# Kernel tuning notes

Measured on AMD Instinct MI355X. Metric: run time of the kernel, lower is better.

Reference implementation:

```python
import jax, jax.numpy as jnp
import numpy as np

NEG = -9e15
EPS = 1e-5

# GraphAttention (classic GAT layer): h = xW; e_ij = LeakyReLU(a1.h_i + a2.h_j);
# attention = softmax(where(adj>0, e, -9e15)); out = attention @ h.
# The torch code builds one big block-diagonal adjacency; off-block entries get
# -9e15 and underflow to exactly 0 after softmax, so batched per-block GAT is
# numerically identical and avoids the O((B*N)^2) dense waste.

def gat(x, adj, W, a1, a2):
    h = jnp.einsum('bnf,fh->bnh', x, W)
    e = jax.nn.leaky_relu(jnp.einsum('bnh,h->bn', h, a1)[:, :, None]
                          + jnp.einsum('bnh,h->bn', h, a2)[:, None, :], 0.2)
    att = jax.nn.softmax(jnp.where(adj > 0, e, NEG), axis=-1)
    return jnp.einsum('bnm,bmh->bnh', att, h)

def mlp(x, W1, b1, W2, b2):
    return jax.nn.relu(x @ W1 + b1) @ W2 + b2


def setup_inputs() -> dict:
    key = jax.random.key(0)
    ks = iter(jax.random.split(key, 40))
    B, NV, NO = 8, 500, 1500
    DV, DO, H = 512, 32, 128

    def mat(din, dout):
        return jax.random.normal(next(ks), (din, dout), jnp.float32) / np.sqrt(din)

    def vec(d):
        return jax.random.normal(next(ks), (d,), jnp.float32) * 0.1

    inp = {
        'vis_memory': jax.random.normal(next(ks), (B, NV, DV), jnp.float32),
        'obj_memory': jax.random.normal(next(ks), (B, NO, DO), jnp.float32),
        'vis_adj': jax.random.uniform(next(ks), (B, NV, NV), jnp.float32),
        'obj_adj': jax.random.uniform(next(ks), (B, NO, NO), jnp.float32),
        'object_A_OV': jax.random.uniform(next(ks), (B, NO, NV), jnp.float32),
        # GAT layers
        'Wv1': mat(DV, H), 'av1a': vec(H), 'av1b': vec(H),
        'Wv2': mat(H, H),  'av2a': vec(H), 'av2b': vec(H),
        'Wo1': mat(DO, H), 'ao1a': vec(H), 'ao1b': vec(H),
        'Wo2': mat(H, H),  'ao2a': vec(H), 'ao2b': vec(H),
        # globalTobject / objectTglobal MLPs
        'g2o_W1': mat(H, H), 'g2o_b1': jnp.zeros((H,), jnp.float32),
        'g2o_W2': mat(H, H), 'g2o_b2': jnp.zeros((H,), jnp.float32),
        'o2g_W1': mat(H, H), 'o2g_b1': jnp.zeros((H,), jnp.float32),
        'o2g_W2': mat(H, H), 'o2g_b2': jnp.zeros((H,), jnp.float32),
        # output projections
        'img_W': mat(H, DV), 'img_b': jnp.zeros((DV,), jnp.float32),
        'obj_W': mat(H, DO), 'obj_b': jnp.zeros((DO,), jnp.float32),
    }
    return inp


def reference(vis_memory, obj_memory, vis_adj, obj_adj, object_A_OV,
              Wv1, av1a, av1b, Wv2, av2a, av2b,
              Wo1, ao1a, ao1b, Wo2, ao2a, ao2b,
              g2o_W1, g2o_b1, g2o_W2, g2o_b2,
              o2g_W1, o2g_b1, o2g_W2, o2g_b2,
              img_W, img_b, obj_W, obj_b):
    # cross adjacencies (block-diagonal in torch -> batched here)
    vo = jnp.swapaxes(object_A_OV, 1, 2)            # (B, NV, NO)
    vo = vo / (vo.sum(2, keepdims=True) + EPS)
    ov = jnp.swapaxes(vo, 1, 2)                     # (B, NO, NV)
    ov = ov / (ov.sum(2, keepdims=True) + EPS)

    v1 = jax.nn.relu(gat(vis_memory, vis_adj, Wv1, av1a, av1b))
    o1 = jax.nn.relu(gat(obj_memory, obj_adj, Wo1, ao1a, ao1b))
    vis = v1 + mlp(jnp.einsum('bvo,boh->bvh', vo, o1), o2g_W1, o2g_b1, o2g_W2, o2g_b2)
    obj = o1 + mlp(jnp.einsum('bov,bvh->boh', ov, v1), g2o_W1, g2o_b1, g2o_W2, g2o_b2)

    v2 = jax.nn.relu(gat(vis, vis_adj, Wv2, av2a, av2b))
    o2 = jax.nn.relu(gat(obj, obj_adj, Wo2, ao2a, ao2b))
    vis = v2 + mlp(jnp.einsum('bvo,boh->bvh', vo, o2), o2g_W1, o2g_b1, o2g_W2, o2g_b2)
    obj = o2 + mlp(jnp.einsum('bov,bvh->boh', ov, v2), g2o_W1, g2o_b1, g2o_W2, g2o_b2)

    vis_out = vis @ img_W + img_b                   # (B, NV, DV)
    obj_out = obj @ obj_W + obj_b                   # (B, NO, DO)
    return (vis_out, obj_out)
```

## Files before the change

### kernel.cpp

```cpp
#include <hip/hip_runtime.h>
#include <math.h>

#define EPSV 1e-5f
#define HD 128
#define IT 64
#define JT 32
#define WP 68
#define CCH 16
#define THR 256

typedef __attribute__((address_space(3))) uint32_t lds_u32_t;
typedef __attribute__((address_space(1))) uint32_t gbl_u32_t;
typedef __attribute__((ext_vector_type(8))) short bf16x8;
typedef __attribute__((ext_vector_type(4))) float f32x4;

__device__ __forceinline__ void async_copy16(const float* g, float* l) {
    __builtin_amdgcn_global_load_lds((const gbl_u32_t*)g, (lds_u32_t*)l, 16, 0, 0);
}

__device__ __forceinline__ void stage_tile_async(const float* gsrc, float* lds, int t) {
    int wv = t >> 6, lane = t & 63;
#pragma unroll
    for (int it = 0; it < 4; ++it) {
        int c = it * 4 + wv;
        async_copy16(gsrc + c * 256 + lane * 4, lds + c * 256);
    }
}

__device__ __forceinline__ void stage_8k_128(const void* g, void* l, int t) {
    const float* gf = (const float*)g; float* lf = (float*)l;
    async_copy16(gf + t * 4, lf + t * 4);
    async_copy16(gf + t * 4 + 512, lf + t * 4 + 512);
    async_copy16(gf + t * 4 + 1024, lf + t * 4 + 1024);
    async_copy16(gf + t * 4 + 1536, lf + t * 4 + 1536);
}

__device__ __forceinline__ unsigned int f2bf(float f) {
    return __builtin_bit_cast(unsigned int, f) >> 16;
}

__device__ __forceinline__ unsigned short rne_bf16(float f) {
    unsigned int u = __builtin_bit_cast(unsigned int, f);
    u += 0x7FFFu + ((u >> 16) & 1u);
    return (unsigned short)(u >> 16);
}

struct WprepP { const float *W, *a1, *a2; unsigned short* WT; float *wa1, *wa2; int K; };
struct XprepP { const float* X; unsigned short* Xbf; const float *wa1, *wa2;
                float *sa, *sb; int rows; };
struct GmfP   { const unsigned short *Xbf, *WT; unsigned short* hT; int N, tilesJ; };
struct AggP  { const unsigned int* mask; const float *sa, *sb, *sm; const unsigned short* hT;
               float* out; int N, tiles, tilesJ; };
struct CrossP{ const float *A, *src, *rs1; float *pp; int iN, jN, tiles, tps; };
struct MlpP  { const float *pp, *scale; int S; const float *W1, *b1, *W2, *b2, *res;
               float *out; int rows; };


__global__ void colsum_part_k(const float* __restrict__ A, float* __restrict__ s1p,
                              int B, int NO, int NV) {
    int v = blockIdx.x * 256 + threadIdx.x;
    int c = blockIdx.y, b = blockIdx.z;
    if (v >= NV) return;
    int chunk = (NO + CCH - 1) / CCH;
    int o0 = c * chunk;
    int o1 = o0 + chunk; if (o1 > NO) o1 = NO;
    const float* Ab = A + (size_t)b * NO * NV + v;
    float s = 0.f;
    for (int o = o0; o < o1; ++o) s += Ab[(size_t)o * NV];
    s1p[((size_t)b * CCH + c) * NV + v] = s;
}

__global__ void colsum_fin_k(const float* __restrict__ s1p, float* __restrict__ rs1,
                             int B, int NV) {
    int idx = blockIdx.x * 256 + threadIdx.x;
    if (idx >= B * NV) return;
    int b = idx / NV, v = idx - b * NV;
    float s = 0.f;
    for (int c = 0; c < CCH; ++c) s += s1p[((size_t)b * CCH + c) * NV + v];
    rs1[idx] = 1.f / (s + EPSV);
}

__global__ void rowsum_inv_k(const float* __restrict__ A, const float* __restrict__ rs1,
                             float* __restrict__ rs2, int B, int NO, int NV) {
    int row = blockIdx.x * (blockDim.x >> 6) + (threadIdx.x >> 6);
    int lane = threadIdx.x & 63;
    if (row >= B * NO) return;
    int b = row / NO;
    const float* Ar = A + (size_t)row * NV;
    const float* r1 = rs1 + (size_t)b * NV;
    float s = 0.f;
    for (int v = lane; v < NV; v += 64) s += Ar[v] * r1[v];
    for (int off = 32; off; off >>= 1) s += __shfl_xor(s, off, 64);
    if (lane == 0) rs2[row] = 1.f / (s + EPSV);
}

template<int N, int TILESJ>
__global__ __launch_bounds__(256)
void maskg_k(const float* __restrict__ adj, unsigned int* __restrict__ maskT) {
    int tid = blockIdx.x * 256 + threadIdx.x;
    int w = tid % TILESJ;
    int rowid = tid / TILESJ;
    if (rowid >= 8 * N) return;
    int b = rowid / N, i = rowid - b * N;
    int j0 = w * 32;
    const float* src = adj + (size_t)rowid * N + j0;
    unsigned int bits = 0u;
    if (j0 + 32 <= N) {
#pragma unroll
        for (int q = 0; q < 8; ++q) {
            float4 v = ((const float4*)src)[q];
            bits |= (v.x > 0.f ? 1u : 0u) << (q * 4 + 0);
            bits |= (v.y > 0.f ? 1u : 0u) << (q * 4 + 1);
            bits |= (v.z > 0.f ? 1u : 0u) << (q * 4 + 2);
            bits |= (v.w > 0.f ? 1u : 0u) << (q * 4 + 3);
        }
    } else {
#pragma unroll
        for (int r = 0; r < 32; ++r)
            if (j0 + r < N) bits |= (src[r] > 0.f ? 1u : 0u) << r;
    }
    maskT[((size_t)b * TILESJ + w) * N + i] = bits;
}

__global__ __launch_bounds__(256)
void wprep_k(WprepP p0, WprepP p1, WprepP p2, WprepP p3, int e0, int e1, int e2) {
    __shared__ float lw[32][129];
    __shared__ float a1s[128], a2s[128];
    int bid = blockIdx.x;
    const WprepP& P = bid < e0 ? p0 : bid < e1 ? p1 : bid < e2 ? p2 : p3;
    int lb = bid < e0 ? bid : bid < e1 ? bid - e0 : bid < e2 ? bid - e1 : bid - e2;
    int k0 = lb * 32, K = P.K;
    int t = threadIdx.x;
    if (t < 128) { a1s[t] = P.a1[t]; a2s[t] = P.a2[t]; }
    for (int idx = t; idx < 32 * 32; idx += 256) {
        int kk = idx >> 5, c4 = idx & 31;
        float4 v = ((const float4*)(P.W + (size_t)(k0 + kk) * 128))[c4];
        lw[kk][c4 * 4 + 0] = v.x; lw[kk][c4 * 4 + 1] = v.y;
        lw[kk][c4 * 4 + 2] = v.z; lw[kk][c4 * 4 + 3] = v.w;
    }
    __syncthreads();
    int kk = t >> 3, g = t & 7;
    float s1 = 0.f, s2 = 0.f;
    for (int c = g; c < 128; c += 8) {
        float w = lw[kk][c];
        s1 = fmaf(w, a1s[c], s1);
        s2 = fmaf(w, a2s[c], s2);
    }
    s1 += __shfl_xor(s1, 1, 64); s1 += __shfl_xor(s1, 2, 64); s1 += __shfl_xor(s1, 4, 64);
    s2 += __shfl_xor(s2, 1, 64); s2 += __shfl_xor(s2, 2, 64); s2 += __shfl_xor(s2, 4, 64);
    if (g == 0) { P.wa1[k0 + kk] = s1; P.wa2[k0 + kk] = s2; }
    for (int idx = t; idx < 4096; idx += 256) {
        int c = idx >> 5, k = idx & 31;
        P.WT[(size_t)c * K + k0 + k] = rne_bf16(lw[k][c]);
    }
}

template<int K>
__device__ void xprep_body(const XprepP& P, int lb) {
    int t = threadIdx.x, wv = t >> 6, lane = t & 63;
    int row = lb * 4 + wv;
    if (row >= P.rows) return;
    const float4* x4 = (const float4*)(P.X + (size_t)row * K);
    const float4* w14 = (const float4*)P.wa1;
    const float4* w24 = (const float4*)P.wa2;
    unsigned short* xb = P.Xbf + (size_t)row * K;
    float s1 = 0.f, s2 = 0.f;
    constexpr int K4 = K / 4;
    constexpr int NI = (K4 + 63) / 64;
#pragma unroll
    for (int i = 0; i < NI; ++i) {
        int k4 = i * 64 + lane;
        if ((K4 % 64 == 0) || (k4 < K4)) {
            float4 x = x4[k4];
            float4 a = w14[k4];
            float4 b = w24[k4];
            s1 += x.x * a.x + x.y * a.y + x.z * a.z + x.w * a.w;
            s2 += x.x * b.x + x.y * b.y + x.z * b.z + x.w * b.w;
            ushort4 p = make_ushort4(rne_bf16(x.x), rne_bf16(x.y),
                                     rne_bf16(x.z), rne_bf16(x.w));
            *(ushort4*)(xb + (size_t)k4 * 4) = p;
        }
    }
#pragma unroll
    for (int off = 32; off; off >>= 1) {
        s1 += __shfl_xor(s1, off, 64);
        s2 += __shfl_xor(s2, off, 64);
    }
    if (lane == 0) { P.sa[row] = s1; P.sb[row] = s2; }
}

template<int KV, int KO>
__global__ __launch_bounds__(256)
void xprep2_k(XprepP V, XprepP O, int GV) {
    int bid = blockIdx.x;
    if (bid < GV) xprep_body<KV>(V, bid);
    else          xprep_body<KO>(O, bid - GV);
}

template<int K>
__device__ void gmf_body(const GmfP& P, int lb) {
    int tilesJ = P.tilesJ, N = P.N;
    int b = lb / tilesJ, jt = lb - b * tilesJ;
    int t = threadIdx.x, wv = t >> 6, lane = t & 63;
    int ml = lane & 15, quad = lane >> 4;
    const unsigned short* xb = P.Xbf + ((size_t)b * N + (size_t)jt * 32) * K;
    const unsigned short* wt0 = P.WT + (size_t)(wv * 32 + ml) * K;
    const unsigned short* wt1 = wt0 + (size_t)16 * K;
    const unsigned short* xb0 = xb + (size_t)ml * K;
    const unsigned short* xb1 = xb + (size_t)(16 + ml) * K;
    f32x4 acc00 = {0.f, 0.f, 0.f, 0.f}, acc01 = acc00, acc10 = acc00, acc11 = acc00;
#pragma unroll 4
    for (int kt = 0; kt < K / 32; ++kt) {
        int kk = kt * 32 + quad * 8;
        bf16x8 a0 = *(const bf16x8*)(wt0 + kk);
        bf16x8 a1 = *(const bf16x8*)(wt1 + kk);
        bf16x8 b0 = *(const bf16x8*)(xb0 + kk);
        bf16x8 b1 = *(const bf16x8*)(xb1 + kk);
        acc00 = __builtin_amdgcn_mfma_f32_16x16x32_bf16(a0, b0, acc00, 0, 0, 0);
        acc01 = __builtin_amdgcn_mfma_f32_16x16x32_bf16(a0, b1, acc01, 0, 0, 0);
        acc10 = __builtin_amdgcn_mfma_f32_16x16x32_bf16(a1, b0, acc10, 0, 0, 0);
        acc11 = __builtin_amdgcn_mfma_f32_16x16x32_bf16(a1, b1, acc11, 0, 0, 0);
    }
    unsigned short* hb = P.hT + (size_t)(b * tilesJ + jt) * 4096;
    int nvalid = N - jt * 32; if (nvalid > 32) nvalid = 32;
    bool ok0 = ml < nvalid, ok1 = (16 + ml) < nvalid;
    int c0 = wv * 32 + quad * 4;
#pragma unroll
    for (int r = 0; r < 4; ++r) {
        int ca = c0 + r, cb = c0 + 16 + r;
        int swa = ((ca >> 1) & 3) << 3, swb = ((cb >> 1) & 3) << 3;
        hb[ca * 32 + (ml ^ swa)]        = ok0 ? rne_bf16(acc00[r]) : 0;
        hb[ca * 32 + ((16 + ml) ^ swa)] = ok1 ? rne_bf16(acc01[r]) : 0;
        hb[cb * 32 + (ml ^ swb)]        = ok0 ? rne_bf16(acc10[r]) : 0;
        hb[cb * 32 + ((16 + ml) ^ swb)] = ok1 ? rne_bf16(acc11[r]) : 0;
    }
}

template<int KV, int KO>
__global__ __launch_bounds__(256)
void gmf2_k(GmfP V, GmfP O, int GV) {
    int bid = blockIdx.x;
    if (bid < GV) gmf_body<KV>(V, bid);
    else          gmf_body<KO>(O, bid - GV);
}

__global__ __launch_bounds__(256)
void sbmax2_k(const float* __restrict__ sbV, float* __restrict__ smV,
              const float* __restrict__ sbO, float* __restrict__ smO,
              int NV, int NO) {
    __shared__ float red[256];
    int b0 = blockIdx.x, t = threadIdx.x;
    const float* sb; float* out; int N;
    if (b0 < 8) { sb = sbV + (size_t)b0 * NV; out = smV + b0; N = NV; }
    else        { sb = sbO + (size_t)(b0 - 8) * NO; out = smO + (b0 - 8); N = NO; }
    float m = -INFINITY;
    for (int j = t; j < N; j += 256) m = fmaxf(m, sb[j]);
    red[t] = m; __syncthreads();
    for (int s = 128; s; s >>= 1) {
        if (t < s) red[t] = fmaxf(red[t], red[t + s]);
        __syncthreads();
    }
    if (t == 0) *out = red[0];
}

struct SharedAgg32 {
    unsigned short hsT[5][128][32];
    unsigned int mask_s[48][32];
    float sb_s[48 * 32];
    float z_s[32];
};

__device__ void agg_body(SharedAgg32& sm, const AggP& P, int lbid) {
    int tiles = P.tiles;
    int b = lbid / tiles;
    int i0 = (lbid - b * tiles) * 32;
    int N = P.N, T = P.tilesJ;
    int t = threadIdx.x;
    int wv = t >> 6, lane = t & 63, quad = lane >> 4, ml = lane & 15;
    const unsigned int* mb = P.mask + (size_t)b * T * N + i0;
    for (int idx = t; idx < T * 8; idx += 128) {
        int w = idx >> 3, r4 = idx & 7;
        *(uint4*)&sm.mask_s[w][r4 * 4] = *(const uint4*)&mb[(size_t)w * N + r4 * 4];
    }
    const float* sbb = P.sb + (size_t)b * N;
    for (int idx = t; idx < T * 8; idx += 128)
        ((float4*)sm.sb_s)[idx] = ((const float4*)sbb)[idx];
    int row_loc = wv * 16 + ml;
    int irow = i0 + row_loc;
    float sa = (irow < N) ? P.sa[(size_t)b * N + irow] : 0.f;
    float e0 = sa + P.sm[b];
    float m = e0 > 0.f ? e0 : 0.2f * e0;
    __syncthreads();
    const unsigned short* hTb = P.hT + (size_t)b * T * 4096;
    stage_8k_128(hTb, &sm.hsT[0][0][0], t);
    if (T > 1) stage_8k_128(hTb + 4096, &sm.hsT[1][0][0], t);
    if (T > 2) stage_8k_128(hTb + 8192, &sm.hsT[2][0][0], t);
    if (T > 3) stage_8k_128(hTb + 12288, &sm.hsT[3][0][0], t);

    int nq2 = (quad ^ ((ml >> 1) & 3)) * 8;
    f32x4 acc[8];
#pragma unroll
    for (int nt = 0; nt < 8; ++nt)
#pragma unroll
        for (int r = 0; r < 4; ++r) acc[nt][r] = 0.f;
    float zacc = 0.f;
    for (int tt = 0; tt < T; ++tt) {
        int cur = tt - (tt / 5) * 5;
        unsigned int mq = sm.mask_s[tt][row_loc] >> (quad * 8);
        float4 s0 = *(const float4*)&sm.sb_s[tt * 32 + quad * 8];
        float4 s1 = *(const float4*)&sm.sb_s[tt * 32 + quad * 8 + 4];
        float sv[8] = {s0.x, s0.y, s0.z, s0.w, s1.x, s1.y, s1.z, s1.w};
        float w_[8];
#pragma unroll
        for (int i = 0; i < 8; ++i) {
            float e = sa + sv[i];
            e = e > 0.f ? e : 0.2f * e;
            float ww = __expf(e - m);
            ww = ((mq >> i) & 1u) ? ww : 0.f;
            zacc += ww;
            w_[i] = ww;
        }
        unsigned int u0 = f2bf(w_[0]) | (__builtin_bit_cast(unsigned int, w_[1]) & 0xFFFF0000u);
        unsigned int u1 = f2bf(w_[2]) | (__builtin_bit_cast(unsigned int, w_[3]) & 0xFFFF0000u);
        unsigned int u2 = f2bf(w_[4]) | (__builtin_bit_cast(unsigned int, w_[5]) & 0xFFFF0000u);
        unsigned int u3 = f2bf(w_[6]) | (__builtin_bit_cast(unsigned int, w_[7]) & 0xFFFF0000u);
        uint4 af = make_uint4(u0, u1, u2, u3);
        bf16x8 afrag = __builtin_bit_cast(bf16x8, af);
        int rem = T - tt;
        if (rem >= 4)      asm volatile("s_waitcnt vmcnt(12)" ::: "memory");
        else if (rem == 3) asm volatile("s_waitcnt vmcnt(8)" ::: "memory");
        else if (rem == 2) asm volatile("s_waitcnt vmcnt(4)" ::: "memory");
        else               asm volatile("s_waitcnt vmcnt(0)" ::: "memory");
        __builtin_amdgcn_s_barrier();
        asm volatile("" ::: "memory");
        if (tt + 4 < T) {
            int nb = tt + 4; nb -= (nb / 5) * 5;
            stage_8k_128(hTb + (size_t)(tt + 4) * 4096, &sm.hsT[nb][0][0], t);
        }
#pragma unroll
        for (int nt = 0; nt < 8; ++nt) {
            bf16x8 bfrag = *(const bf16x8*)&sm.hsT[cur][nt * 16 + ml][nq2];
            acc[nt] = __builtin_amdgcn_mfma_f32_16x16x32_bf16(afrag, bfrag, acc[nt], 0, 0, 0);
        }
    }
    zacc += __shfl_xor(zacc, 16, 64);
    zacc += __shfl_xor(zacc, 32, 64);
    if (quad == 0) sm.z_s[row_loc] = zacc;
    __syncthreads();
    float* outb = P.out + (size_t)b * N * HD;
#pragma unroll
    for (int r = 0; r < 4; ++r) {
        int rr = wv * 16 + quad * 4 + r;
        float inv = 1.f / sm.z_s[rr];
        int row = i0 + rr;
        if (row < N) {
#pragma unroll
            for (int nt = 0; nt < 8; ++nt)
                outb[(size_t)row * HD + nt * 16 + ml] = fmaxf(acc[nt][r] * inv, 0.f);
        }
    }
}

__global__ __launch_bounds__(128)
void agg2_k(AggP V, AggP O, int GVb) {
    __shared__ SharedAgg32 sm;
    int bid = blockIdx.x;
    if (bid < GVb) agg_body(sm, V, bid);
    else           agg_body(sm, O, bid - GVb);
}

__device__ __forceinline__ void tile_fma256(const float (*hs)[HD], const float (*ws)[WP],
                                            int rg, int c0, float acc[4][8]) {
#pragma unroll 8
    for (int jl = 0; jl < JT; ++jl) {
        float4 h0 = *(const float4*)&hs[jl][c0];
        float4 h1 = *(const float4*)&hs[jl][c0 + 64];
        float4 w4 = *(const float4*)&ws[jl][rg * 4];
        float wq[4] = {w4.x, w4.y, w4.z, w4.w};
#pragma unroll
        for (int q = 0; q < 4; ++q) {
            float w = wq[q];
            acc[q][0] = fmaf(w, h0.x, acc[q][0]);
            acc[q][1] = fmaf(w, h0.y, acc[q][1]);
            acc[q][2] = fmaf(w, h0.z, acc[q][2]);
            acc[q][3] = fmaf(w, h0.w, acc[q][3]);
            acc[q][4] = fmaf(w, h1.x, acc[q][4]);
            acc[q][5] = fmaf(w, h1.y, acc[q][5]);
            acc[q][6] = fmaf(w, h1.z, acc[q][6]);
            acc[q][7] = fmaf(w, h1.w, acc[q][7]);
        }
    }
}

__device__ __forceinline__ void part_store256(float* __restrict__ pp, size_t base,
                                              int i0, int N, int rg, int c0,
                                              float acc[4][8]) {
#pragma unroll
    for (int q = 0; q < 4; ++q) {
        int i = i0 + rg * 4 + q;
        if (i >= N) continue;
        float* op = pp + base + (size_t)i * HD;
        *(float4*)&op[c0]      = make_float4(acc[q][0], acc[q][1], acc[q][2], acc[q][3]);
        *(float4*)&op[c0 + 64] = make_float4(acc[q][4], acc[q][5], acc[q][6], acc[q][7]);
    }
}

struct SharedTile { float hs[2][JT][HD]; float ws[2][JT][WP]; };

__device__ void cross_vo_body(SharedTile& sm, const CrossP& P, int lbid) {
    int tiles = P.tiles;
    int split = lbid / (8 * tiles);
    int rem = lbid - split * 8 * tiles;
    int b = rem / tiles;
    int i0 = (rem - b * tiles) * IT;
    int NVl = P.iN, NOl = P.jN;
    int j_begin = split * P.tps * JT;
    if (j_begin >= NOl) return;
    int j_end = j_begin + P.tps * JT;
    if (j_end > NOl) j_end = NOl;
    int T = (j_end - j_begin + JT - 1) / JT;
    int t = threadIdx.x;
    int rg = t >> 4, c0 = (t & 15) * 4;
    int il = t & 63, jlb = t >> 6;
    float acc[4][8];
#pragma unroll
    for (int q = 0; q < 4; ++q)
#pragma unroll
        for (int x = 0; x < 8; ++x) acc[q][x] = 0.f;
    const float* Ab = P.A + (size_t)b * NOl * NVl;
    const float* srcb = P.src + (size_t)b * NOl * HD;
    int v = i0 + il;
    float w8[8];
    stage_tile_async(srcb + (size_t)j_begin * HD, &sm.hs[0][0][0], t);
#pragma unroll
    for (int k = 0; k < 8; ++k) {
        int o = j_begin + jlb + k * 4;
        w8[k] = (v < NVl && o < NOl) ? Ab[(size_t)o * NVl + v] : 0.f;
    }
    for (int tt = 0; tt < T; ++tt) {
        int cur = tt & 1;
#pragma unroll
        for (int k = 0; k < 8; ++k) sm.ws[cur][jlb + k * 4][il] = w8[k];
        __syncthreads();
        if (tt + 1 < T) {
            int jn = j_begin + (tt + 1) * JT;
            stage_tile_async(srcb + (size_t)jn * HD, &sm.hs[1 - cur][0][0], t);
#pragma unroll
            for (int k = 0; k < 8; ++k) {
                int o = jn + jlb + k * 4;
                w8[k] = (v < NVl && o < NOl) ? Ab[(size_t)o * NVl + v] : 0.f;
            }
        }
        tile_fma256(sm.hs[cur], sm.ws[cur], rg, c0, acc);
    }
    size_t rowsTot = (size_t)8 * NVl;
    part_store256(P.pp, ((size_t)split * rowsTot + (size_t)b * NVl) * HD, i0, NVl, rg, c0, acc);
}

__device__ void cross_ov_body(SharedTile& sm, const CrossP& P, int lbid) {
    int tiles = P.tiles;
    int split = lbid / (8 * tiles);
    int rem = lbid - split * 8 * tiles;
    int b = rem / tiles;
    int i0 = (rem - b * tiles) * IT;
    int NOl = P.iN, NVl = P.jN;
    int j_begin = split * P.tps * JT;
    if (j_begin >= NVl) return;
    int j_end = j_begin + P.tps * JT;
    if (j_end > NVl) j_end = NVl;
    int T = (j_end - j_begin + JT - 1) / JT;
    int t = threadIdx.x;
    int rg = t >> 4, c0 = (t & 15) * 4;
    int il = t >> 2, j4 = (t & 3) * 4;
    float acc[4][8];
#pragma unroll
    for (int q = 0; q < 4; ++q)
#pragma unroll
        for (int x = 0; x < 8; ++x) acc[q][x] = 0.f;
    const float* Ab = P.A + (size_t)b * NOl * NVl;
    const float* srcb = P.src + (size_t)b * NVl * HD;
    const float* r1b = P.rs1 + (size_t)b * NVl;
    int orow = i0 + il;
    float4 a4[2], r4[2];
    stage_tile_async(srcb + (size_t)j_begin * HD, &sm.hs[0][0][0], t);
#pragma unroll
    for (int k = 0; k < 2; ++k) {
        int vv = j_begin + j4 + k * 16;
        float4 av = make_float4(0.f,0.f,0.f,0.f), rv = make_float4(0.f,0.f,0.f,0.f);
        if (orow < NOl) {
            if (vv + 3 < NVl) {
                av = *(const float4*)&Ab[(size_t)orow * NVl + vv];
                rv = *(const float4*)&r1b[vv];
            } else {
                float* ap = (float*)&av; float* rp = (float*)&rv;
                for (int r = 0; r < 4; ++r)
                    if (vv + r < NVl) { ap[r] = Ab[(size_t)orow * NVl + vv + r]; rp[r] = r1b[vv + r]; }
            }
        }
        a4[k] = av; r4[k] = rv;
    }
    for (int tt = 0; tt < T; ++tt) {
        int cur = tt & 1;
#pragma unroll
        for (int k = 0; k < 2; ++k) {
            float wv[4] = {a4[k].x * r4[k].x, a4[k].y * r4[k].y,
                           a4[k].z * r4[k].z, a4[k].w * r4[k].w};
#pragma unroll
            for (int r = 0; r < 4; ++r) sm.ws[cur][j4 + r + k * 16][il] = wv[r];
        }
        __syncthreads();
        if (tt + 1 < T) {
            int jn = j_begin + (tt + 1) * JT;
            stage_tile_async(srcb + (size_t)jn * HD, &sm.hs[1 - cur][0][0], t);
#pragma unroll
            for (int k = 0; k < 2; ++k) {
                int vv = jn + j4 + k * 16;
                float4 av = make_float4(0.f,0.f,0.f,0.f), rv = make_float4(0.f,0.f,0.f,0.f);
                if (orow < NOl) {
                    if (vv + 3 < NVl) {
                        av = *(const float4*)&Ab[(size_t)orow * NVl + vv];
                        rv = *(const float4*)&r1b[vv];
                    } else {
                        float* ap = (float*)&av; float* rp = (float*)&rv;
                        for (int r = 0; r < 4; ++r)
                            if (vv + r < NVl) { ap[r] = Ab[(size_t)orow * NVl + vv + r]; rp[r] = r1b[vv + r]; }
                    }
                }
                a4[k] = av; r4[k] = rv;
            }
        }
        tile_fma256(sm.hs[cur], sm.ws[cur], rg, c0, acc);
    }
    size_t rowsTot = (size_t)8 * NOl;
    part_store256(P.pp, ((size_t)split * rowsTot + (size_t)b * NOl) * HD, i0, NOl, rg, c0, acc);
}

__global__ __launch_bounds__(256)
void cross2_k(CrossP VO, CrossP OV, int GVOb) {
    __shared__ SharedTile sm;
    int bid = blockIdx.x;
    if (bid < GVOb) cross_vo_body(sm, VO, bid);
    else            cross_ov_body(sm, OV, bid - GVOb);
}

__global__ __launch_bounds__(128)
void mlp2_k(MlpP V, MlpP O, int GVb) {
    __shared__ float xs[8][HD];
    __shared__ float hh[8][HD];
    int bid = blockIdx.x;
    const MlpP& P = (bid < GVb) ? V : O;
    int row0 = ((bid < GVb) ? bid : bid - GVb) * 8;
    int rows = P.rows;
    int t = threadIdx.x;
    for (int l = t; l < 8 * 32; l += 128) {
        int r = l >> 5, c4 = l & 31;
        int row = row0 + r;
        float4 v = make_float4(0.f, 0.f, 0.f, 0.f);
        if (row < rows) {
            for (int s = 0; s < P.S; ++s) {
                float4 p = ((const float4*)P.pp)[((size_t)s * rows + row) * 32 + c4];
                v.x += p.x; v.y += p.y; v.z += p.z; v.w += p.w;
            }
            float sc = P.scale[row];
            v.x *= sc; v.y *= sc; v.z *= sc; v.w *= sc;
        }
        ((float4*)&xs[r][0])[c4] = v;
    }
    __syncthreads();
    int wv = t >> 6, tt = t & 63, rb = wv * 4;
    float a0[4] = {0.f, 0.f, 0.f, 0.f}, a1v[4] = {0.f, 0.f, 0.f, 0.f};
#pragma unroll 4
    for (int k = 0; k < HD; ++k) {
        float w0 = P.W1[(size_t)k * HD + tt];
        float w1 = P.W1[(size_t)k * HD + tt + 64];
#pragma unroll
        for (int r = 0; r < 4; ++r) {
            float x = xs[rb + r][k];
            a0[r] = fmaf(x, w0, a0[r]);
            a1v[r] = fmaf(x, w1, a1v[r]);
        }
    }
    float bb0 = P.b1[tt], bb1 = P.b1[tt + 64];
#pragma unroll
    for (int r = 0; r < 4; ++r) {
        hh[rb + r][tt]      = fmaxf(a0[r] + bb0, 0.f);
        hh[rb + r][tt + 64] = fmaxf(a1v[r] + bb1, 0.f);
    }
    __syncthreads();
    float c0a[4] = {0.f, 0.f, 0.f, 0.f}, c1a[4] = {0.f, 0.f, 0.f, 0.f};
#pragma unroll 4
    for (int k = 0; k < HD; ++k) {
        float w0 = P.W2[(size_t)k * HD + tt];
        float w1 = P.W2[(size_t)k * HD + tt + 64];
#pragma unroll
        for (int r = 0; r < 4; ++r) {
            float x = hh[rb + r][k];
            c0a[r] = fmaf(x, w0, c0a[r]);
            c1a[r] = fmaf(x, w1, c1a[r]);
        }
    }
    float d0 = P.b2[tt], d1 = P.b2[tt + 64];
#pragma unroll
    for (int r = 0; r < 4; ++r) {
        int row = row0 + rb + r;
        if (row >= rows) continue;
        P.out[(size_t)row * HD + tt]      = c0a[r] + d0 + P.res[(size_t)row * HD + tt];
        P.out[(size_t)row * HD + tt + 64] = c1a[r] + d1 + P.res[(size_t)row * HD + tt + 64];
    }
}

template<int RELU, int BIAS, int RES>
__global__ __launch_bounds__(128)
void linear_k(const float* __restrict__ X, const float* __restrict__ W,
              const float* __restrict__ bias, const float* __restrict__ res,
              float* __restrict__ out, int rows, int K, int Dout) {
    __shared__ float xs[4][512];
    int row0 = blockIdx.x * 4;
    int t = threadIdx.x;
    int K4 = K >> 2;
    for (int l = t; l < 4 * K4; l += 128) {
        int r = l / K4, c4 = l - r * K4;
        float4 val = make_float4(0.f, 0.f, 0.f, 0.f);
        if (row0 + r < rows) val = ((const float4*)(X + (size_t)(row0 + r) * K))[c4];
        ((float4*)&xs[r][0])[c4] = val;
    }
    __syncthreads();
    int chunk = Dout < 256 ? Dout : 256;
    int half = chunk >> 1;
    if (t >= half) return;
    int c0 = blockIdx.y * chunk + t;
    int c1 = c0 + half;
    float a00 = 0, a01 = 0, a02 = 0, a03 = 0, a10 = 0, a11 = 0, a12 = 0, a13 = 0;
#pragma unroll 4
    for (int k = 0; k < K; ++k) {
        float w0 = W[(size_t)k * Dout + c0];
        float w1 = W[(size_t)k * Dout + c1];
        float x0 = xs[0][k], x1 = xs[1][k], x2 = xs[2][k], x3 = xs[3][k];
        a00 = fmaf(x0, w0, a00); a01 = fmaf(x1, w0, a01);
        a02 = fmaf(x2, w0, a02); a03 = fmaf(x3, w0, a03);
        a10 = fmaf(x0, w1, a10); a11 = fmaf(x1, w1, a11);
        a12 = fmaf(x2, w1, a12); a13 = fmaf(x3, w1, a13);
    }
    float accs[2][4] = {{a00, a01, a02, a03}, {a10, a11, a12, a13}};
    int cs[2] = {c0, c1};
    for (int h = 0; h < 2; ++h) {
        float bv = BIAS ? bias[cs[h]] : 0.f;
        for (int r = 0; r < 4; ++r) {
            int row = row0 + r;
            if (row >= rows) continue;
            float v = accs[h][r] + bv;
            if (RES) v += res[(size_t)row * Dout + cs[h]];
            if (RELU) v = fmaxf(v, 0.f);
            out[(size_t)row * Dout + cs[h]] = v;
        }
    }
}

extern "C" void kernel_launch(void* const* d_in, const int* in_sizes, int n_in,
                              void* d_out, int out_size, void* d_ws, size_t ws_size,
                              hipStream_t stream) {
    const int B = 8, NV = 500, NO = 1500, DV = 512, DO = 32;
    const float* vis_memory = (const float*)d_in[0];
    const float* obj_memory = (const float*)d_in[1];
    const float* vis_adj    = (const float*)d_in[2];
    const float* obj_adj    = (const float*)d_in[3];
    const float* A_OV       = (const float*)d_in[4];
    const float* Wv1  = (const float*)d_in[5];
    const float* av1a = (const float*)d_in[6];
    const float* av1b = (const float*)d_in[7];
    const float* Wv2  = (const float*)d_in[8];
    const float* av2a = (const float*)d_in[9];
    const float* av2b = (const float*)d_in[10];
    const float* Wo1  = (const float*)d_in[11];
    const float* ao1a = (const float*)d_in[12];
    const float* ao1b = (const float*)d_in[13];
    const float* Wo2  = (const float*)d_in[14];
    const float* ao2a = (const float*)d_in[15];
    const float* ao2b = (const float*)d_in[16];
    const float* g2o_W1 = (const float*)d_in[17];
    const float* g2o_b1 = (const float*)d_in[18];
    const float* g2o_W2 = (const float*)d_in[19];
    const float* g2o_b2 = (const float*)d_in[20];
    const float* o2g_W1 = (const float*)d_in[21];
    const float* o2g_b1 = (const float*)d_in[22];
    const float* o2g_W2 = (const float*)d_in[23];
    const float* o2g_b2 = (const float*)d_in[24];
    const float* img_W = (const float*)d_in[25];
    const float* img_b = (const float*)d_in[26];
    const float* obj_W = (const float*)d_in[27];
    const float* obj_b = (const float*)d_in[28];

    const int tilesJV = 16, tilesJO = 47;

    float* wsp = (float*)d_ws;
    size_t off = 0;
    auto alloc = [&](size_t n) { float* p = wsp + off; off += (n + 3) & ~(size_t)3; return p; };
    float* rs1   = alloc(B * NV);
    float* rs2   = alloc(B * NO);
    float* saV   = alloc(B * NV);
    float* sbV   = alloc(B * NV);
    float* smV   = alloc(B);
    float* saO   = alloc(B * NO);
    float* sbO   = alloc(B * NO);
    float* smO   = alloc(B);
    float* s1p   = alloc((size_t)B * CCH * NV);
    unsigned int* maskV = (unsigned int*)alloc((size_t)B * tilesJV * NV);
    unsigned int* maskO = (unsigned int*)alloc((size_t)B * tilesJO * NO);
    unsigned short* WTv1 = (unsigned short*)alloc(128 * 512 / 2);
    unsigned short* WTo1 = (unsigned short*)alloc(128 * 32 / 2);
    unsigned short* WTv2 = (unsigned short*)alloc(128 * 128 / 2);
    unsigned short* WTo2 = (unsigned short*)alloc(128 * 128 / 2);
    float* wav1a = alloc(512); float* wav1b = alloc(512);
    float* wao1a = alloc(32);  float* wao1b = alloc(32);
    float* wav2a = alloc(128); float* wav2b = alloc(128);
    float* wao2a = alloc(128); float* wao2b = alloc(128);
    unsigned short* XbfV = (unsigned short*)alloc((size_t)B * NV * 512 / 2);
    unsigned short* XbfO = (unsigned short*)alloc((size_t)B * NO * 128 / 2);
    unsigned short* hTv = (unsigned short*)alloc((size_t)B * tilesJV * 4096 / 2);
    unsigned short* hTo = (unsigned short*)alloc((size_t)B * tilesJO * 4096 / 2);
    float* v1    = alloc((size_t)B * NV * HD);
    float* o1    = alloc((size_t)B * NO * HD);
    float* visb  = alloc((size_t)B * NV * HD);
    float* objb  = alloc((size_t)B * NO * HD);
    float* ppV   = alloc((size_t)8 * B * NV * HD);
    float* ppO   = alloc((size_t)4 * B * NO * HD);
    alloc(16384);

    {
        WprepP w0{Wv1, av1a, av1b, WTv1, wav1a, wav1b, DV};
        WprepP w1{Wo1, ao1a, ao1b, WTo1, wao1a, wao1b, DO};
        WprepP w2{Wv2, av2a, av2b, WTv2, wav2a, wav2b, HD};
        WprepP w3{Wo2, ao2a, ao2b, WTo2, wao2a, wao2b, HD};
        wprep_k<<<25, 256, 0, stream>>>(w0, w1, w2, w3, 16, 17, 21);
    }
    maskg_k<500, 16><<<(8 * 500 * 16 + 255) / 256, 256, 0, stream>>>(vis_adj, maskV);
    maskg_k<1500, 47><<<(8 * 1500 * 47 + 255) / 256, 256, 0, stream>>>(obj_adj, maskO);

    colsum_part_k<<<dim3((NV + 255) / 256, CCH, B), 256, 0, stream>>>(A_OV, s1p, B, NO, NV);
    colsum_fin_k<<<dim3((B * NV + 255) / 256), 256, 0, stream>>>(s1p, rs1, B, NV);
    rowsum_inv_k<<<dim3((B * NO + 3) / 4), 256, 0, stream>>>(A_OV, rs1, rs2, B, NO, NV);

    const int tilesV32 = 16, tilesO32 = 47;
    const int tilesV = 8, tilesO = 24;
    const int SVO = 8, SOV = 4;
    const int tpsVO = 6;
    const int tpsOV = 4;
    const int G_AGG_V = B * tilesV32;
    const int G_AGG_O = B * tilesO32;
    const int G_CR_VO = B * tilesV * SVO;
    const int G_CR_OV = B * tilesO * SOV;
    const int G_MLP_V = B * NV / 8;
    const int G_MLP_O = B * NO / 8;
    const int G_XP_V = B * NV / 4;
    const int G_XP_O = B * NO / 4;
    const int G_GMF_V = B * tilesJV;
    const int G_GMF_O = B * tilesJO;

    auto tail = [&](float* visout, float* objout) {
        sbmax2_k<<<16, 256, 0, stream>>>(sbV, smV, sbO, smO, NV, NO);
        AggP av{maskV, saV, sbV, smV, hTv, v1, NV, tilesV32, tilesJV};
        AggP ao{maskO, saO, sbO, smO, hTo, o1, NO, tilesO32, tilesJO};
        agg2_k<<<G_AGG_V + G_AGG_O, 128, 0, stream>>>(av, ao, G_AGG_V);
        CrossP cvo{A_OV, o1, nullptr, ppV, NV, NO, tilesV, tpsVO};
        CrossP cov{A_OV, v1, rs1, ppO, NO, NV, tilesO, tpsOV};
        cross2_k<<<G_CR_VO + G_CR_OV, THR, 0, stream>>>(cvo, cov, G_CR_VO);
        MlpP mv{ppV, rs1, SVO, o2g_W1, o2g_b1, o2g_W2, o2g_b2, v1, visout, B * NV};
        MlpP mo{ppO, rs2, SOV, g2o_W1, g2o_b1, g2o_W2, g2o_b2, o1, objout, B * NO};
        mlp2_k<<<G_MLP_V + G_MLP_O, 128, 0, stream>>>(mv, mo, G_MLP_V);
    };

    {
        XprepP xv{vis_memory, XbfV, wav1a, wav1b, saV, sbV, B * NV};
        XprepP xo{obj_memory, XbfO, wao1a, wao1b, saO, sbO, B * NO};
        xprep2_k<512, 32><<<G_XP_V + G_XP_O, 256, 0, stream>>>(xv, xo, G_XP_V);
        GmfP gv{XbfV, WTv1, hTv, NV, tilesJV};
        GmfP go{XbfO, WTo1, hTo, NO, tilesJO};
        gmf2_k<512, 32><<<G_GMF_V + G_GMF_O, 256, 0, stream>>>(gv, go, G_GMF_V);
        tail(visb, objb);
    }
    {
        XprepP xv{visb, XbfV, wav2a, wav2b, saV, sbV, B * NV};
        XprepP xo{objb, XbfO, wao2a, wao2b, saO, sbO, B * NO};
        xprep2_k<128, 128><<<G_XP_V + G_XP_O, 256, 0, stream>>>(xv, xo, G_XP_V);
        GmfP gv{XbfV, WTv2, hTv, NV, tilesJV};
        GmfP go{XbfO, WTo2, hTo, NO, tilesJO};
        gmf2_k<128, 128><<<G_GMF_V + G_GMF_O, 256, 0, stream>>>(gv, go, G_GMF_V);
        tail(visb, objb);
    }

    float* vis_out = (float*)d_out;
    float* obj_out = vis_out + (size_t)B * NV * DV;
    linear_k<0, 1, 0><<<dim3((B * NV + 3) / 4, (DV + 255) / 256), 128, 0, stream>>>(
        visb, img_W, img_b, nullptr, vis_out, B * NV, HD, DV);
    linear_k<0, 1, 0><<<dim3((B * NO + 3) / 4, 1), 128, 0, stream>>>(
        objb, obj_W, obj_b, nullptr, obj_out, B * NO, HD, DO);
}
```

Before: 589.0 us.

## Move cross-adjacency matmuls to bf16 MFMA with fused pre-transposed operand export

The cross vis/obj aggregation kernels are rewritten from FP32 FMA tiles with split-K partial buffers to bf16 MFMA tiles that loop over the full reduction with a 5-deep async LDS pipeline. The GAT aggregation kernel now also writes its output as swizzled, transposed bf16 tiles, pre-scaled by rs1 for the vis path, so the cross kernels can read them directly. The split-K partial sums and the MLP's scale step are dropped, and the row scaling is applied in the cross epilogue. This reduces FP32 compute and partial-buffer traffic, but the A_OV weights and aggregated features are rounded to bf16, and there are fewer blocks with longer loops.

```diff
diff --git a/kernel.cpp b/kernel.cpp
--- a/kernel.cpp
+++ b/kernel.cpp
@@ -3,11 +3,7 @@
 
 #define EPSV 1e-5f
 #define HD 128
-#define IT 64
-#define JT 32
-#define WP 68
 #define CCH 16
-#define THR 256
 
 typedef __attribute__((address_space(3))) uint32_t lds_u32_t;
 typedef __attribute__((address_space(1))) uint32_t gbl_u32_t;
@@ -16,15 +12,6 @@
 
 __device__ __forceinline__ void async_copy16(const float* g, float* l) {
     __builtin_amdgcn_global_load_lds((const gbl_u32_t*)g, (lds_u32_t*)l, 16, 0, 0);
-}
-
-__device__ __forceinline__ void stage_tile_async(const float* gsrc, float* lds, int t) {
-    int wv = t >> 6, lane = t & 63;
-#pragma unroll
-    for (int it = 0; it < 4; ++it) {
-        int c = it * 4 + wv;
-        async_copy16(gsrc + c * 256 + lane * 4, lds + c * 256);
-    }
 }
 
 __device__ __forceinline__ void stage_8k_128(const void* g, void* l, int t) {
@@ -45,13 +32,23 @@
     return (unsigned short)(u >> 16);
 }
 
+__device__ __forceinline__ bf16x8 pack8_rne(const float* w) {
+    unsigned int u0 = (unsigned int)rne_bf16(w[0]) | ((unsigned int)rne_bf16(w[1]) << 16);
+    unsigned int u1 = (unsigned int)rne_bf16(w[2]) | ((unsigned int)rne_bf16(w[3]) << 16);
+    unsigned int u2 = (unsigned int)rne_bf16(w[4]) | ((unsigned int)rne_bf16(w[5]) << 16);
+    unsigned int u3 = (unsigned int)rne_bf16(w[6]) | ((unsigned int)rne_bf16(w[7]) << 16);
+    uint4 af = make_uint4(u0, u1, u2, u3);
+    return __builtin_bit_cast(bf16x8, af);
+}
+
 struct WprepP { const float *W, *a1, *a2; unsigned short* WT; float *wa1, *wa2; int K; };
 struct XprepP { const float* X; unsigned short* Xbf; const float *wa1, *wa2;
                 float *sa, *sb; int rows; };
 struct GmfP   { const unsigned short *Xbf, *WT; unsigned short* hT; int N, tilesJ; };
 struct AggP  { const unsigned int* mask; const float *sa, *sb, *sm; const unsigned short* hT;
-               float* out; int N, tiles, tilesJ; };
-struct CrossP{ const float *A, *src, *rs1; float *pp; int iN, jN, tiles, tps; };
+               float* out; unsigned short* hTout; const float* rsc; int N, tiles, tilesJ; };
+struct CrossP{ const float* A; const unsigned short* hT; const float* rs_row;
+               float* out; int iN, jN, tilesI, T; };
 struct MlpP  { const float *pp, *scale; int S; const float *W1, *b1, *W2, *b2, *res;
                float *out; int rows; };
 
@@ -273,7 +270,8 @@
 __device__ void agg_body(SharedAgg32& sm, const AggP& P, int lbid) {
     int tiles = P.tiles;
     int b = lbid / tiles;
-    int i0 = (lbid - b * tiles) * 32;
+    int jt_i = lbid - b * tiles;
+    int i0 = jt_i * 32;
     int N = P.N, T = P.tilesJ;
     int t = threadIdx.x;
     int wv = t >> 6, lane = t & 63, quad = lane >> 4, ml = lane & 15;
@@ -348,15 +346,22 @@
     if (quad == 0) sm.z_s[row_loc] = zacc;
     __syncthreads();
     float* outb = P.out + (size_t)b * N * HD;
+    unsigned short* hb = P.hTout + ((size_t)b * tiles + jt_i) * 4096;
 #pragma unroll
     for (int r = 0; r < 4; ++r) {
         int rr = wv * 16 + quad * 4 + r;
         float inv = 1.f / sm.z_s[rr];
         int row = i0 + rr;
-        if (row < N) {
-#pragma unroll
-            for (int nt = 0; nt < 8; ++nt)
-                outb[(size_t)row * HD + nt * 16 + ml] = fmaxf(acc[nt][r] * inv, 0.f);
+        bool ok = row < N;
+        float sc = 1.f;
+        if (P.rsc != nullptr && ok) sc = P.rsc[(size_t)b * N + row];
+#pragma unroll
+        for (int nt = 0; nt < 8; ++nt) {
+            float val = fmaxf(acc[nt][r] * inv, 0.f);
+            if (ok) outb[(size_t)row * HD + nt * 16 + ml] = val;
+            int c = nt * 16 + ml;
+            int sw = ((c >> 1) & 3) << 3;
+            hb[c * 32 + (rr ^ sw)] = ok ? rne_bf16(val * sc) : (unsigned short)0;
         }
     }
 }
@@ -369,175 +374,145 @@
     else           agg_body(sm, O, bid - GVb);
 }
 
-__device__ __forceinline__ void tile_fma256(const float (*hs)[HD], const float (*ws)[WP],
-                                            int rg, int c0, float acc[4][8]) {
-#pragma unroll 8
-    for (int jl = 0; jl < JT; ++jl) {
-        float4 h0 = *(const float4*)&hs[jl][c0];
-        float4 h1 = *(const float4*)&hs[jl][c0 + 64];
-        float4 w4 = *(const float4*)&ws[jl][rg * 4];
-        float wq[4] = {w4.x, w4.y, w4.z, w4.w};
-#pragma unroll
-        for (int q = 0; q < 4; ++q) {
-            float w = wq[q];
-            acc[q][0] = fmaf(w, h0.x, acc[q][0]);
-            acc[q][1] = fmaf(w, h0.y, acc[q][1]);
-            acc[q][2] = fmaf(w, h0.z, acc[q][2]);
-            acc[q][3] = fmaf(w, h0.w, acc[q][3]);
-            acc[q][4] = fmaf(w, h1.x, acc[q][4]);
-            acc[q][5] = fmaf(w, h1.y, acc[q][5]);
-            acc[q][6] = fmaf(w, h1.z, acc[q][6]);
-            acc[q][7] = fmaf(w, h1.w, acc[q][7]);
-        }
-    }
-}
-
-__device__ __forceinline__ void part_store256(float* __restrict__ pp, size_t base,
-                                              int i0, int N, int rg, int c0,
-                                              float acc[4][8]) {
-#pragma unroll
-    for (int q = 0; q < 4; ++q) {
-        int i = i0 + rg * 4 + q;
-        if (i >= N) continue;
-        float* op = pp + base + (size_t)i * HD;
-        *(float4*)&op[c0]      = make_float4(acc[q][0], acc[q][1], acc[q][2], acc[q][3]);
-        *(float4*)&op[c0 + 64] = make_float4(acc[q][4], acc[q][5], acc[q][6], acc[q][7]);
-    }
-}
-
-struct SharedTile { float hs[2][JT][HD]; float ws[2][JT][WP]; };
-
-__device__ void cross_vo_body(SharedTile& sm, const CrossP& P, int lbid) {
-    int tiles = P.tiles;
-    int split = lbid / (8 * tiles);
-    int rem = lbid - split * 8 * tiles;
-    int b = rem / tiles;
-    int i0 = (rem - b * tiles) * IT;
-    int NVl = P.iN, NOl = P.jN;
-    int j_begin = split * P.tps * JT;
-    if (j_begin >= NOl) return;
-    int j_end = j_begin + P.tps * JT;
-    if (j_end > NOl) j_end = NOl;
-    int T = (j_end - j_begin + JT - 1) / JT;
-    int t = threadIdx.x;
-    int rg = t >> 4, c0 = (t & 15) * 4;
-    int il = t & 63, jlb = t >> 6;
-    float acc[4][8];
-#pragma unroll
-    for (int q = 0; q < 4; ++q)
-#pragma unroll
-        for (int x = 0; x < 8; ++x) acc[q][x] = 0.f;
-    const float* Ab = P.A + (size_t)b * NOl * NVl;
-    const float* srcb = P.src + (size_t)b * NOl * HD;
-    int v = i0 + il;
-    float w8[8];
-    stage_tile_async(srcb + (size_t)j_begin * HD, &sm.hs[0][0][0], t);
-#pragma unroll
-    for (int k = 0; k < 8; ++k) {
-        int o = j_begin + jlb + k * 4;
-        w8[k] = (v < NVl && o < NOl) ? Ab[(size_t)o * NVl + v] : 0.f;
-    }
-    for (int tt = 0; tt < T; ++tt) {
-        int cur = tt & 1;
-#pragma unroll
-        for (int k = 0; k < 8; ++k) sm.ws[cur][jlb + k * 4][il] = w8[k];
-        __syncthreads();
-        if (tt + 1 < T) {
-            int jn = j_begin + (tt + 1) * JT;
-            stage_tile_async(srcb + (size_t)jn * HD, &sm.hs[1 - cur][0][0], t);
-#pragma unroll
-            for (int k = 0; k < 8; ++k) {
-                int o = jn + jlb + k * 4;
-                w8[k] = (v < NVl && o < NOl) ? Ab[(size_t)o * NVl + v] : 0.f;
-            }
-        }
-        tile_fma256(sm.hs[cur], sm.ws[cur], rg, c0, acc);
-    }
-    size_t rowsTot = (size_t)8 * NVl;
-    part_store256(P.pp, ((size_t)split * rowsTot + (size_t)b * NVl) * HD, i0, NVl, rg, c0, acc);
-}
-
-__device__ void cross_ov_body(SharedTile& sm, const CrossP& P, int lbid) {
-    int tiles = P.tiles;
-    int split = lbid / (8 * tiles);
-    int rem = lbid - split * 8 * tiles;
-    int b = rem / tiles;
-    int i0 = (rem - b * tiles) * IT;
-    int NOl = P.iN, NVl = P.jN;
-    int j_begin = split * P.tps * JT;
-    if (j_begin >= NVl) return;
-    int j_end = j_begin + P.tps * JT;
-    if (j_end > NVl) j_end = NVl;
-    int T = (j_end - j_begin + JT - 1) / JT;
-    int t = threadIdx.x;
-    int rg = t >> 4, c0 = (t & 15) * 4;
-    int il = t >> 2, j4 = (t & 3) * 4;
-    float acc[4][8];
-#pragma unroll
-    for (int q = 0; q < 4; ++q)
-#pragma unroll
-        for (int x = 0; x < 8; ++x) acc[q][x] = 0.f;
-    const float* Ab = P.A + (size_t)b * NOl * NVl;
-    const float* srcb = P.src + (size_t)b * NVl * HD;
-    const float* r1b = P.rs1 + (size_t)b * NVl;
-    int orow = i0 + il;
-    float4 a4[2], r4[2];
-    stage_tile_async(srcb + (size_t)j_begin * HD, &sm.hs[0][0][0], t);
-#pragma unroll
-    for (int k = 0; k < 2; ++k) {
-        int vv = j_begin + j4 + k * 16;
-        float4 av = make_float4(0.f,0.f,0.f,0.f), rv = make_float4(0.f,0.f,0.f,0.f);
-        if (orow < NOl) {
-            if (vv + 3 < NVl) {
-                av = *(const float4*)&Ab[(size_t)orow * NVl + vv];
-                rv = *(const float4*)&r1b[vv];
-            } else {
-                float* ap = (float*)&av; float* rp = (float*)&rv;
-                for (int r = 0; r < 4; ++r)
-                    if (vv + r < NVl) { ap[r] = Ab[(size_t)orow * NVl + vv + r]; rp[r] = r1b[vv + r]; }
-            }
-        }
-        a4[k] = av; r4[k] = rv;
-    }
-    for (int tt = 0; tt < T; ++tt) {
-        int cur = tt & 1;
-#pragma unroll
-        for (int k = 0; k < 2; ++k) {
-            float wv[4] = {a4[k].x * r4[k].x, a4[k].y * r4[k].y,
-                           a4[k].z * r4[k].z, a4[k].w * r4[k].w};
-#pragma unroll
-            for (int r = 0; r < 4; ++r) sm.ws[cur][j4 + r + k * 16][il] = wv[r];
-        }
-        __syncthreads();
-        if (tt + 1 < T) {
-            int jn = j_begin + (tt + 1) * JT;
-            stage_tile_async(srcb + (size_t)jn * HD, &sm.hs[1 - cur][0][0], t);
-#pragma unroll
-            for (int k = 0; k < 2; ++k) {
-                int vv = jn + j4 + k * 16;
-                float4 av = make_float4(0.f,0.f,0.f,0.f), rv = make_float4(0.f,0.f,0.f,0.f);
-                if (orow < NOl) {
-                    if (vv + 3 < NVl) {
-                        av = *(const float4*)&Ab[(size_t)orow * NVl + vv];
-                        rv = *(const float4*)&r1b[vv];
-                    } else {
-                        float* ap = (float*)&av; float* rp = (float*)&rv;
-                        for (int r = 0; r < 4; ++r)
-                            if (vv + r < NVl) { ap[r] = Ab[(size_t)orow * NVl + vv + r]; rp[r] = r1b[vv + r]; }
-                    }
-                }
-                a4[k] = av; r4[k] = rv;
-            }
-        }
-        tile_fma256(sm.hs[cur], sm.ws[cur], rg, c0, acc);
-    }
-    size_t rowsTot = (size_t)8 * NOl;
-    part_store256(P.pp, ((size_t)split * rowsTot + (size_t)b * NOl) * HD, i0, NOl, rg, c0, acc);
-}
-
-__global__ __launch_bounds__(256)
+struct SharedCr { unsigned short hsT[5][128][32]; };
+
+__device__ void cross_vo_body(SharedCr& sm, const CrossP& P, int lbid) {
+    int tiles = P.tilesI;
+    int b = lbid / tiles;
+    int i0 = (lbid - b * tiles) * 32;
+    int iN = P.iN, jN = P.jN, T = P.T;
+    int t = threadIdx.x, wv = t >> 6, lane = t & 63, quad = lane >> 4, ml = lane & 15;
+    int row_loc = wv * 16 + ml;
+    int irow = i0 + row_loc;
+    int ivc = irow < iN ? irow : iN - 1;
+    const float* Ab = P.A + (size_t)b * jN * iN;
+    const unsigned short* hTb = P.hT + (size_t)b * T * 4096;
+    float wA[8], wB[8];
+#define VO_LOAD(W_, jt_) do { int _o0 = (jt_) * 32 + quad * 8;                     \
+    _Pragma("unroll") for (int _i = 0; _i < 8; ++_i) {                             \
+        int _o = _o0 + _i; _o = _o < jN ? _o : jN - 1;                             \
+        W_[_i] = Ab[(size_t)_o * iN + ivc]; } } while (0)
+    stage_8k_128(hTb,            &sm.hsT[0][0][0], t); VO_LOAD(wA, 0);
+    stage_8k_128(hTb + 4096,     &sm.hsT[1][0][0], t); VO_LOAD(wB, 0);
+    stage_8k_128(hTb + 2 * 4096, &sm.hsT[2][0][0], t); VO_LOAD(wA, 0);
+    stage_8k_128(hTb + 3 * 4096, &sm.hsT[3][0][0], t); VO_LOAD(wB, 1);
+    int nq2 = (quad ^ ((ml >> 1) & 3)) * 8;
+    f32x4 acc[8];
+#pragma unroll
+    for (int nt = 0; nt < 8; ++nt)
+#pragma unroll
+        for (int r = 0; r < 4; ++r) acc[nt][r] = 0.f;
+#define CR_VO_TILE(tt_, W_) do {                                                   \
+    bf16x8 afrag_ = pack8_rne(W_);                                                 \
+     \
+    asm volatile("s_waitcnt vmcnt(44)" ::: "memory");                              \
+    __builtin_amdgcn_s_barrier();                                                  \
+    asm volatile("" ::: "memory");                                                 \
+    { int _srct = (tt_) + 4 < T ? (tt_) + 4 : T - 1;                               \
+      int _dbuf = (tt_) + 4; _dbuf -= (_dbuf / 5) * 5;                             \
+      stage_8k_128(hTb + (size_t)_srct * 4096, &sm.hsT[_dbuf][0][0], t); }         \
+    { int _at = (tt_) + 2 < T ? (tt_) + 2 : T - 1;                                 \
+      VO_LOAD(W_, _at); }                                                          \
+    { int _cur = (tt_); _cur -= (_cur / 5) * 5;                                    \
+      _Pragma("unroll")                                                            \
+      for (int nt = 0; nt < 8; ++nt) {                                             \
+          bf16x8 bfrag_ = *(const bf16x8*)&sm.hsT[_cur][nt * 16 + ml][nq2];        \
+          acc[nt] = __builtin_amdgcn_mfma_f32_16x16x32_bf16(afrag_, bfrag_, acc[nt], 0, 0, 0); \
+      } }                                                                          \
+} while (0)
+    int tt = 0;
+    while (true) {
+        CR_VO_TILE(tt, wA); ++tt; if (tt >= T) break;
+        CR_VO_TILE(tt, wB); ++tt; if (tt >= T) break;
+    }
+#undef CR_VO_TILE
+#undef VO_LOAD
+    asm volatile("s_waitcnt vmcnt(0)" ::: "memory");
+    float* outb = P.out + (size_t)b * iN * HD;
+#pragma unroll
+    for (int r = 0; r < 4; ++r) {
+        int rr = wv * 16 + quad * 4 + r;
+        int row = i0 + rr;
+        if (row < iN) {
+            float s = P.rs_row[(size_t)b * iN + row];
+#pragma unroll
+            for (int nt = 0; nt < 8; ++nt)
+                outb[(size_t)row * HD + nt * 16 + ml] = acc[nt][r] * s;
+        }
+    }
+}
+
+__device__ void cross_ov_body(SharedCr& sm, const CrossP& P, int lbid) {
+    int tiles = P.tilesI;
+    int b = lbid / tiles;
+    int i0 = (lbid - b * tiles) * 32;
+    int iN = P.iN, jN = P.jN, T = P.T;
+    int t = threadIdx.x, wv = t >> 6, lane = t & 63, quad = lane >> 4, ml = lane & 15;
+    int row_loc = wv * 16 + ml;
+    int irow = i0 + row_loc;
+    int ivc = irow < iN ? irow : iN - 1;
+    const float* Ab = P.A + (size_t)b * iN * jN;
+    const unsigned short* hTb = P.hT + (size_t)b * T * 4096;
+    float wA[8], wB[8];
+#define OV_LOAD(W_, jt_) do { int _v0 = (jt_) * 32 + quad * 8;                     \
+    _v0 = _v0 + 8 <= jN ? _v0 : jN - 8;                                            \
+    const float* _p = Ab + (size_t)ivc * jN + _v0;                                 \
+    float4 _a = *(const float4*)_p; float4 _c = *(const float4*)(_p + 4);          \
+    W_[0] = _a.x; W_[1] = _a.y; W_[2] = _a.z; W_[3] = _a.w;                        \
+    W_[4] = _c.x; W_[5] = _c.y; W_[6] = _c.z; W_[7] = _c.w; } while (0)
+    stage_8k_128(hTb,            &sm.hsT[0][0][0], t); OV_LOAD(wA, 0);
+    stage_8k_128(hTb + 4096,     &sm.hsT[1][0][0], t); OV_LOAD(wB, 0);
+    stage_8k_128(hTb + 2 * 4096, &sm.hsT[2][0][0], t); OV_LOAD(wA, 0);
+    stage_8k_128(hTb + 3 * 4096, &sm.hsT[3][0][0], t); OV_LOAD(wB, 1);
+    int nq2 = (quad ^ ((ml >> 1) & 3)) * 8;
+    f32x4 acc[8];
+#pragma unroll
+    for (int nt = 0; nt < 8; ++nt)
+#pragma unroll
+        for (int r = 0; r < 4; ++r) acc[nt][r] = 0.f;
+#define CR_OV_TILE(tt_, W_) do {                                                   \
+    bf16x8 afrag_ = pack8_rne(W_);                                                 \
+                        \
+    asm volatile("s_waitcnt vmcnt(20)" ::: "memory");                              \
+    __builtin_amdgcn_s_barrier();                                                  \
+    asm volatile("" ::: "memory");                                                 \
+    { int _srct = (tt_) + 4 < T ? (tt_) + 4 : T - 1;                               \
+      int _dbuf = (tt_) + 4; _dbuf -= (_dbuf / 5) * 5;                             \
+      stage_8k_128(hTb + (size_t)_srct * 4096, &sm.hsT[_dbuf][0][0], t); }         \
+    { int _at = (tt_) + 2 < T ? (tt_) + 2 : T - 1;                                 \
+      OV_LOAD(W_, _at); }                                                          \
+    { int _cur = (tt_); _cur -= (_cur / 5) * 5;                                    \
+      _Pragma("unroll")                                                            \
+      for (int nt = 0; nt < 8; ++nt) {                                             \
+          bf16x8 bfrag_ = *(const bf16x8*)&sm.hsT[_cur][nt * 16 + ml][nq2];        \
+          acc[nt] = __builtin_amdgcn_mfma_f32_16x16x32_bf16(afrag_, bfrag_, acc[nt], 0, 0, 0); \
+      } }                                                                          \
+} while (0)
+    int tt = 0;
+    while (true) {
+        CR_OV_TILE(tt, wA); ++tt; if (tt >= T) break;
+        CR_OV_TILE(tt, wB); ++tt; if (tt >= T) break;
+    }
+#undef CR_OV_TILE
+#undef OV_LOAD
+    asm volatile("s_waitcnt vmcnt(0)" ::: "memory");
+    float* outb = P.out + (size_t)b * iN * HD;
+#pragma unroll
+    for (int r = 0; r < 4; ++r) {
+        int rr = wv * 16 + quad * 4 + r;
+        int row = i0 + rr;
+        if (row < iN) {
+            float s = P.rs_row[(size_t)b * iN + row];
+#pragma unroll
+            for (int nt = 0; nt < 8; ++nt)
+                outb[(size_t)row * HD + nt * 16 + ml] = acc[nt][r] * s;
+        }
+    }
+}
+
+__global__ __launch_bounds__(128)
 void cross2_k(CrossP VO, CrossP OV, int GVOb) {
-    __shared__ SharedTile sm;
+    __shared__ SharedCr sm;
     int bid = blockIdx.x;
     if (bid < GVOb) cross_vo_body(sm, VO, bid);
     else            cross_ov_body(sm, OV, bid - GVOb);
@@ -561,8 +536,10 @@
                 float4 p = ((const float4*)P.pp)[((size_t)s * rows + row) * 32 + c4];
                 v.x += p.x; v.y += p.y; v.z += p.z; v.w += p.w;
             }
-            float sc = P.scale[row];
-            v.x *= sc; v.y *= sc; v.z *= sc; v.w *= sc;
+            if (P.scale != nullptr) {
+                float sc = P.scale[row];
+                v.x *= sc; v.y *= sc; v.z *= sc; v.w *= sc;
+            }
         }
         ((float4*)&xs[r][0])[c4] = v;
     }
@@ -718,12 +695,14 @@
     unsigned short* XbfO = (unsigned short*)alloc((size_t)B * NO * 128 / 2);
     unsigned short* hTv = (unsigned short*)alloc((size_t)B * tilesJV * 4096 / 2);
     unsigned short* hTo = (unsigned short*)alloc((size_t)B * tilesJO * 4096 / 2);
+    unsigned short* hTv2 = (unsigned short*)alloc((size_t)B * tilesJV * 4096 / 2);
+    unsigned short* hTo2 = (unsigned short*)alloc((size_t)B * tilesJO * 4096 / 2);
     float* v1    = alloc((size_t)B * NV * HD);
     float* o1    = alloc((size_t)B * NO * HD);
     float* visb  = alloc((size_t)B * NV * HD);
     float* objb  = alloc((size_t)B * NO * HD);
-    float* ppV   = alloc((size_t)8 * B * NV * HD);
-    float* ppO   = alloc((size_t)4 * B * NO * HD);
+    float* ppV   = alloc((size_t)B * NV * HD);
+    float* ppO   = alloc((size_t)B * NO * HD);
     alloc(16384);
 
     {
@@ -740,15 +719,10 @@
     colsum_fin_k<<<dim3((B * NV + 255) / 256), 256, 0, stream>>>(s1p, rs1, B, NV);
     rowsum_inv_k<<<dim3((B * NO + 3) / 4), 256, 0, stream>>>(A_OV, rs1, rs2, B, NO, NV);
 
-    const int tilesV32 = 16, tilesO32 = 47;
-    const int tilesV = 8, tilesO = 24;
-    const int SVO = 8, SOV = 4;
-    const int tpsVO = 6;
-    const int tpsOV = 4;
-    const int G_AGG_V = B * tilesV32;
-    const int G_AGG_O = B * tilesO32;
-    const int G_CR_VO = B * tilesV * SVO;
-    const int G_CR_OV = B * tilesO * SOV;
+    const int G_AGG_V = B * tilesJV;
+    const int G_AGG_O = B * tilesJO;
+    const int G_CR_VO = B * tilesJV;
+    const int G_CR_OV = B * tilesJO;
     const int G_MLP_V = B * NV / 8;
     const int G_MLP_O = B * NO / 8;
     const int G_XP_V = B * NV / 4;
@@ -758,14 +732,14 @@
 
     auto tail = [&](float* visout, float* objout) {
         sbmax2_k<<<16, 256, 0, stream>>>(sbV, smV, sbO, smO, NV, NO);
-        AggP av{maskV, saV, sbV, smV, hTv, v1, NV, tilesV32, tilesJV};
-        AggP ao{maskO, saO, sbO, smO, hTo, o1, NO, tilesO32, tilesJO};
+        AggP av{maskV, saV, sbV, smV, hTv, v1, hTv2, rs1, NV, tilesJV, tilesJV};
+        AggP ao{maskO, saO, sbO, smO, hTo, o1, hTo2, nullptr, NO, tilesJO, tilesJO};
         agg2_k<<<G_AGG_V + G_AGG_O, 128, 0, stream>>>(av, ao, G_AGG_V);
-        CrossP cvo{A_OV, o1, nullptr, ppV, NV, NO, tilesV, tpsVO};
-        CrossP cov{A_OV, v1, rs1, ppO, NO, NV, tilesO, tpsOV};
-        cross2_k<<<G_CR_VO + G_CR_OV, THR, 0, stream>>>(cvo, cov, G_CR_VO);
-        MlpP mv{ppV, rs1, SVO, o2g_W1, o2g_b1, o2g_W2, o2g_b2, v1, visout, B * NV};
-        MlpP mo{ppO, rs2, SOV, g2o_W1, g2o_b1, g2o_W2, g2o_b2, o1, objout, B * NO};
+        CrossP cvo{A_OV, hTo2, rs1, ppV, NV, NO, tilesJV, tilesJO};
+        CrossP cov{A_OV, hTv2, rs2, ppO, NO, NV, tilesJO, tilesJV};
+        cross2_k<<<G_CR_VO + G_CR_OV, 128, 0, stream>>>(cvo, cov, G_CR_VO);
+        MlpP mv{ppV, nullptr, 1, o2g_W1, o2g_b1, o2g_W2, o2g_b2, v1, visout, B * NV};
+        MlpP mo{ppO, nullptr, 1, g2o_W1, g2o_b1, g2o_W2, g2o_b2, o1, objout, B * NO};
         mlp2_k<<<G_MLP_V + G_MLP_O, 128, 0, stream>>>(mv, mo, G_MLP_V);
     };
 
```

New measurement: 529.5 us. -10.1%, faster.
